# Kernel optimization log

Hardware: AMD Instinct MI355X
Metric: run time of the kernel (lower is better)

The kernel has to match this reference:

```python
import jax, jax.numpy as jnp
import numpy as np
from jax import lax

B, T, Z, H, F = 64, 256, 128, 512, 64
EPS = 1e-3  # keras LayerNormalization default epsilon


def _glorot(key, shape):
    fan_in, fan_out = shape[0], shape[1]
    lim = np.sqrt(6.0 / (fan_in + fan_out)).astype(np.float32)
    return jax.random.uniform(key, shape, jnp.float32, -lim, lim)


def setup_inputs() -> dict:
    key = jax.random.key(0)
    ks = jax.random.split(key, 16)
    inp = {
        "z": jax.random.normal(ks[0], (B, T, Z), jnp.float32),
        "Wp": _glorot(ks[1], (Z, 2 * H)), "bp": jnp.zeros((2 * H,), jnp.float32),
        "Ws": _glorot(ks[2], (Z, H)), "bs": jnp.zeros((H,), jnp.float32),
        "K0": _glorot(ks[3], (2 * H, 4 * H)), "R0": _glorot(ks[4], (H, 4 * H)), "b0": jnp.zeros((4 * H,), jnp.float32),
        "K1": _glorot(ks[5], (H, 4 * H)), "R1": _glorot(ks[6], (H, 4 * H)), "b1": jnp.zeros((4 * H,), jnp.float32),
        "K2": _glorot(ks[7], (H, 4 * H)), "R2": _glorot(ks[8], (H, 4 * H)), "b2": jnp.zeros((4 * H,), jnp.float32),
        "gamma": jnp.ones((H,), jnp.float32), "beta": jnp.zeros((H,), jnp.float32),
        "W1": _glorot(ks[9], (H, H)), "b1d": jnp.zeros((H,), jnp.float32),
        "W2": _glorot(ks[10], (H, F)), "b2d": jnp.zeros((F,), jnp.float32),
    }
    return inp


def _lstm(x, K, R, b):
    # x: [B, T, D]; keras gate order i, f, g(c), o
    xK = jnp.swapaxes(jnp.einsum('btd,dg->btg', x, K) + b, 0, 1)  # [T, B, 4H]
    h0 = jnp.zeros((x.shape[0], H), x.dtype)
    c0 = jnp.zeros((x.shape[0], H), x.dtype)

    def step(carry, xk):
        h, c = carry
        zg = xk + h @ R
        i, f, g, o = jnp.split(zg, 4, axis=-1)
        c = jax.nn.sigmoid(f) * c + jax.nn.sigmoid(i) * jnp.tanh(g)
        h = jax.nn.sigmoid(o) * jnp.tanh(c)
        return (h, c), h

    _, hs = lax.scan(step, (h0, c0), xK)
    return jnp.swapaxes(hs, 0, 1)  # [B, T, H]


def reference(z, Wp, bp, Ws, bs, K0, R0, b0, K1, R1, b1, K2, R2, b2,
              gamma, beta, W1, b1d, W2, b2d):
    x = jnp.einsum('btz,zd->btd', z, Wp) + bp          # dense_proj -> [B,T,2H]
    residual = jnp.einsum('btz,zh->bth', z, Ws) + bs   # skip_proj  -> [B,T,H]
    x = _lstm(x, K0, R0, b0)
    x = _lstm(x, K1, R1, b1)
    x = x + residual  # use_residual, after layer index 1
    x = _lstm(x, K2, R2, b2)
    # training=False: dropout is identity and attention branch is skipped
    mu = jnp.mean(x, axis=-1, keepdims=True)
    var = jnp.mean(jnp.square(x - mu), axis=-1, keepdims=True)
    x = (x - mu) * lax.rsqrt(var + EPS) * gamma + beta
    x = jax.nn.relu(jnp.einsum('bth,hk->btk', x, W1) + b1d)
    x = jnp.tanh(jnp.einsum('bth,hf->btf', x, W2) + b2d)
    return x
```

## Files before the change

kernel.cpp:

```cpp
#include <hip/hip_runtime.h>
#include <hip/hip_fp16.h>
#include <stdint.h>

typedef unsigned short u16;
typedef unsigned int   u32;
typedef unsigned long long u64;
typedef __attribute__((ext_vector_type(8))) short s16x8;
typedef __attribute__((ext_vector_type(8))) _Float16 h16x8;
typedef __attribute__((ext_vector_type(4))) float f32x4;

#define T_LEN 256

__device__ __forceinline__ u16 f2h(float f){ return __half_as_ushort(__float2half(f)); }
__device__ __forceinline__ float h2f(u16 x){ union{u16 u; _Float16 h;} c; c.u = x; return (float)c.h; }
__device__ __forceinline__ h16x8 as_h(s16x8 v){ union{s16x8 s; h16x8 h;} u; u.s=v; return u.h; }
__device__ __forceinline__ float sigm(float x){ return 1.f/(1.f + __expf(-x)); }
__device__ __forceinline__ float tanh_f(float x){ return 2.f*sigm(2.f*x) - 1.f; }

__global__ void k_fuse(const float* __restrict__ Wp, const float* __restrict__ K0,
                       const float* __restrict__ Ws, const float* __restrict__ K2,
                       float* __restrict__ Wf0, float* __restrict__ Wf2)
{
  const int c  = blockIdx.x*256 + threadIdx.x;
  const int by = blockIdx.y;
  float acc[8] = {0,0,0,0,0,0,0,0};
  if (by < 16){
    const int r0 = by*8;
    for (int d = 0; d < 1024; ++d){
      float kv = K0[(size_t)d*2048 + c];
      #pragma unroll
      for (int ii = 0; ii < 8; ++ii) acc[ii] = fmaf(Wp[(size_t)(r0+ii)*1024 + d], kv, acc[ii]);
    }
    #pragma unroll
    for (int ii = 0; ii < 8; ++ii) Wf0[(size_t)(r0+ii)*2048 + c] = acc[ii];
  } else {
    const int r0 = (by-16)*8;
    for (int u = 0; u < 512; ++u){
      float kv = K2[(size_t)u*2048 + c];
      #pragma unroll
      for (int ii = 0; ii < 8; ++ii) acc[ii] = fmaf(Ws[(size_t)(r0+ii)*512 + u], kv, acc[ii]);
    }
    #pragma unroll
    for (int ii = 0; ii < 8; ++ii) Wf2[(size_t)(r0+ii)*2048 + c] = acc[ii];
  }
}

__global__ void k_bias(const float* __restrict__ bp, const float* __restrict__ K0,
                       const float* __restrict__ b0, const float* __restrict__ bs,
                       const float* __restrict__ K2, const float* __restrict__ b2,
                       float* __restrict__ gb0, float* __restrict__ gb2)
{
  const int bx = blockIdx.x;
  if (bx < 8){
    int c = bx*256 + threadIdx.x;
    float a = b0[c];
    for (int d = 0; d < 1024; ++d) a = fmaf(bp[d], K0[(size_t)d*2048 + c], a);
    gb0[c] = a;
  } else {
    int c = (bx-8)*256 + threadIdx.x;
    float a = b2[c];
    for (int u = 0; u < 512; ++u) a = fmaf(bs[u], K2[(size_t)u*2048 + c], a);
    gb2[c] = a;
  }
}

__global__ void k_zero(u32* __restrict__ hfz, int* __restrict__ flags)
{
  int idx = blockIdx.x*256 + threadIdx.x;
  if (idx < 49152){
    int L = idx >> 14, off = idx & 16383;
    hfz[(size_t)L*257*16384 + off] = 0u;
  }
  if (blockIdx.x == 0 && threadIdx.x < 192) flags[threadIdx.x] = -1;
}

__device__ __forceinline__ size_t gidx(int k, int c, int K32c){
  int gate = c >> 9, u = c & 511;
  int jj = u >> 3, uu = u & 7;
  int lc = gate*8 + uu;
  return ((size_t)(jj*2 + (lc>>4))*K32c + (k>>5))*512
         + (size_t)((((k>>3)&3)*16 + (lc&15))*8) + (size_t)(k&7);
}
__device__ __forceinline__ size_t fidx(int k, int c){
  return ((size_t)(c>>4)*16 + (k>>5))*512
         + (size_t)((((k>>3)&3)*16 + (c&15))*8) + (size_t)(k&7);
}

__global__ void k_pack(const float* __restrict__ R0, const float* __restrict__ Wf0,
                       const float* __restrict__ R1, const float* __restrict__ K1,
                       const float* __restrict__ R2, const float* __restrict__ K2,
                       const float* __restrict__ Wf2, const float* __restrict__ W1,
                       const float* __restrict__ W2, const float* __restrict__ z,
                       u16* __restrict__ wgt0, u16* __restrict__ wgt1, u16* __restrict__ wgt2,
                       u16* __restrict__ w1p,  u16* __restrict__ w2p,  u16* __restrict__ zp)
{
  const long NT = 8159232;
  for (long i = (long)blockIdx.x*256 + threadIdx.x; i < NT; i += (long)gridDim.x*256){
    if (i < 1310720){
      int k = (int)(i >> 11), c = (int)(i & 2047);
      float v = (k < 512) ? R0[(size_t)k*2048 + c] : Wf0[(size_t)(k-512)*2048 + c];
      wgt0[gidx(k, c, 20)] = f2h(v);
    } else if (i < 3407872){
      long i2 = i - 1310720; int k = (int)(i2 >> 11), c = (int)(i2 & 2047);
      float v = (k < 512) ? R1[(size_t)k*2048 + c] : K1[(size_t)(k-512)*2048 + c];
      wgt1[gidx(k, c, 32)] = f2h(v);
    } else if (i < 5767168){
      long i2 = i - 3407872; int k = (int)(i2 >> 11), c = (int)(i2 & 2047);
      float v = (k < 512)  ? R2[(size_t)k*2048 + c]
              : (k < 1024) ? K2[(size_t)(k-512)*2048 + c]
                           : Wf2[(size_t)(k-1024)*2048 + c];
      wgt2[gidx(k, c, 36)] = f2h(v);
    } else if (i < 6029312){
      long i2 = i - 5767168; int k = (int)(i2 >> 9), c = (int)(i2 & 511);
      w1p[fidx(k, c)] = f2h(W1[(size_t)k*512 + c]);
    } else if (i < 6062080){
      long i2 = i - 6029312; int k = (int)(i2 >> 6), c = (int)(i2 & 63);
      w2p[fidx(k, c)] = f2h(W2[(size_t)k*64 + c]);
    } else {
      long i2 = i - 6062080;
      int bb = (int)(i2 >> 15), rem = (int)(i2 & 32767);
      int tt = rem >> 7, k = rem & 127;
      zp[(((size_t)tt*4 + (bb>>4))*4 + (k>>5))*512
         + (size_t)((((k>>3)&3)*16 + (bb&15))*8) + (size_t)(k&7)] = f2h(z[i2]);
    }
  }
}

__global__ __launch_bounds__(256, 1) void k_wave(
    const u16* __restrict__ wgt0, const u16* __restrict__ wgt1, const u16* __restrict__ wgt2,
    const u16* __restrict__ zp, u16* __restrict__ hf, int* flags,
    u64* __restrict__ ackdump, const float* __restrict__ gb0,
    const float* __restrict__ b1g, const float* __restrict__ gb2)
{
  __shared__ __align__(16) u16 wsm[2*36*512];
  __shared__ float zg[64][33];
  __shared__ __align__(16) u16 hsh[64][8];
  const int tid = threadIdx.x;
  const int bid = blockIdx.x;
  const int L   = bid >> 6;
  const int j   = bid & 63;
  const int K32r = (L==0) ? 20 : ((L==1) ? 32 : 36);

  { const u16* wsrc = (L==0) ? wgt0 + (size_t)j*20480
                    : (L==1) ? wgt1 + (size_t)j*32768
                             : wgt2 + (size_t)j*36864;
    const uint4* s4 = (const uint4*)wsrc; uint4* d4 = (uint4*)wsm;
    const int n4 = K32r*128;
    for (int i = tid; i < n4; i += 256) d4[i] = s4[i]; }

  const int b    = tid & 63;
  const int q    = tid >> 6;
  const int w    = q;
  const int lane = tid & 63;

  float bias[2][4];
  { const float* bsrc = (L==0) ? gb0 : (L==1) ? b1g : gb2;
    #pragma unroll
    for (int ci = 0; ci < 2; ++ci){
      int ucol = j*8 + 2*q + ci;
      #pragma unroll
      for (int g = 0; g < 4; ++g) bias[ci][g] = bsrc[g*512 + ucol];
    } }
  float cst0 = 0.f, cst1 = 0.f;
  u64 ackacc = 0;

  const int smt   = tid >> 5;
  const int sbm   = (tid >> 1) & 15;
  const int shalf = tid & 1;
  const size_t schunk = ((size_t)(smt*16 + (j>>2))*64 + ((j&3)*16 + sbm))*8 + shalf*4;

  __syncthreads();

  for (int s = 0; s < T_LEN + 2; ++s){
    if (q == 0){
      const int need = s - 1;
      int g = 0;
      for (;;){
        int okk = (__hip_atomic_load(&flags[L*64 + lane], __ATOMIC_RELAXED,
                                     __HIP_MEMORY_SCOPE_AGENT) >= need);
        if (L > 0)
          okk &= (__hip_atomic_load(&flags[(L-1)*64 + lane], __ATOMIC_RELAXED,
                                    __HIP_MEMORY_SCOPE_AGENT) >= need);
        if (__all(okk) || ++g > (1<<20)) break;
        __builtin_amdgcn_s_sleep(2);
      }
    }
    __syncthreads();

    const int t = s - L;
    if (t >= 0 && t < T_LEN){
      f32x4 acc0 = {0.f,0.f,0.f,0.f};
      f32x4 acc1 = {0.f,0.f,0.f,0.f};
      const size_t wl8 = (size_t)w*8192 + (size_t)lane*8;
      const u16* hself = hf + ((size_t)(L*257 + t))*32768 + wl8;
      const u16* hblw  = (L > 0) ? hf + ((size_t)((L-1)*257 + t + 1))*32768 + wl8 : nullptr;
      const u16* zpt   = zp + (size_t)t*8192 + (size_t)w*2048 + (size_t)lane*8;

      if (L == 0){
        s16x8 areg[20];
        #pragma unroll
        for (int kk = 0; kk < 16; ++kk) areg[kk]    = *(const s16x8*)(hself + (size_t)kk*512);
        #pragma unroll
        for (int kk = 0; kk < 4; ++kk)  areg[16+kk] = *(const s16x8*)(zpt   + (size_t)kk*512);
        #pragma unroll
        for (int kk = 0; kk < 20; ++kk){
          h16x8 bv0 = as_h(*(const s16x8*)&wsm[kk*512 + lane*8]);
          h16x8 bv1 = as_h(*(const s16x8*)&wsm[(20+kk)*512 + lane*8]);
          acc0 = __builtin_amdgcn_mfma_f32_16x16x32_f16(as_h(areg[kk]), bv0, acc0, 0, 0, 0);
          acc1 = __builtin_amdgcn_mfma_f32_16x16x32_f16(as_h(areg[kk]), bv1, acc1, 0, 0, 0);
        }
      } else if (L == 1){
        s16x8 areg[32];
        #pragma unroll
        for (int kk = 0; kk < 16; ++kk) areg[kk]    = *(const s16x8*)(hself + (size_t)kk*512);
        #pragma unroll
        for (int kk = 0; kk < 16; ++kk) areg[16+kk] = *(const s16x8*)(hblw  + (size_t)kk*512);
        #pragma unroll
        for (int kk = 0; kk < 32; ++kk){
          h16x8 bv0 = as_h(*(const s16x8*)&wsm[kk*512 + lane*8]);
          h16x8 bv1 = as_h(*(const s16x8*)&wsm[(32+kk)*512 + lane*8]);
          acc0 = __builtin_amdgcn_mfma_f32_16x16x32_f16(as_h(areg[kk]), bv0, acc0, 0, 0, 0);
          acc1 = __builtin_amdgcn_mfma_f32_16x16x32_f16(as_h(areg[kk]), bv1, acc1, 0, 0, 0);
        }
      } else {
        s16x8 areg[36];
        #pragma unroll
        for (int kk = 0; kk < 16; ++kk) areg[kk]    = *(const s16x8*)(hself + (size_t)kk*512);
        #pragma unroll
        for (int kk = 0; kk < 16; ++kk) areg[16+kk] = *(const s16x8*)(hblw  + (size_t)kk*512);
        #pragma unroll
        for (int kk = 0; kk < 4; ++kk)  areg[32+kk] = *(const s16x8*)(zpt   + (size_t)kk*512);
        #pragma unroll
        for (int kk = 0; kk < 36; ++kk){
          h16x8 bv0 = as_h(*(const s16x8*)&wsm[kk*512 + lane*8]);
          h16x8 bv1 = as_h(*(const s16x8*)&wsm[(36+kk)*512 + lane*8]);
          acc0 = __builtin_amdgcn_mfma_f32_16x16x32_f16(as_h(areg[kk]), bv0, acc0, 0, 0, 0);
          acc1 = __builtin_amdgcn_mfma_f32_16x16x32_f16(as_h(areg[kk]), bv1, acc1, 0, 0, 0);
        }
      }
      #pragma unroll
      for (int r = 0; r < 4; ++r){
        int row = (w << 4) + ((lane >> 4) << 2) + r;
        zg[row][lane & 15]        = acc0[r];
        zg[row][16 + (lane & 15)] = acc1[r];
      }
      __syncthreads();

      float hv0, hv1;
      {
        int uu = 2*q;
        float zi = zg[b][uu]      + bias[0][0];
        float zf = zg[b][8 + uu]  + bias[0][1];
        float zc = zg[b][16 + uu] + bias[0][2];
        float zo = zg[b][24 + uu] + bias[0][3];
        float cc = sigm(zf)*cst0 + sigm(zi)*tanh_f(zc);
        cst0 = cc; hv0 = sigm(zo)*tanh_f(cc);
      }
      {
        int uu = 2*q + 1;
        float zi = zg[b][uu]      + bias[1][0];
        float zf = zg[b][8 + uu]  + bias[1][1];
        float zc = zg[b][16 + uu] + bias[1][2];
        float zo = zg[b][24 + uu] + bias[1][3];
        float cc = sigm(zf)*cst1 + sigm(zi)*tanh_f(zc);
        cst1 = cc; hv1 = sigm(zo)*tanh_f(cc);
      }
      *(u32*)&hsh[b][2*q] = (u32)f2h(hv0) | ((u32)f2h(hv1) << 16);
      __syncthreads();
      if (tid < 128){
        u16* hdst = hf + ((size_t)(L*257 + t + 1))*32768;
        u64 v = *(const u64*)&hsh[smt*16 + sbm][shalf*4];
        u64 old = __hip_atomic_exchange((u64*)(hdst + schunk), v,
                                        __ATOMIC_RELAXED, __HIP_MEMORY_SCOPE_AGENT);
        ackacc ^= old;
      }
    }
    __syncthreads();
    if (tid == 0)
      __hip_atomic_store(&flags[L*64 + j], s, __ATOMIC_RELAXED, __HIP_MEMORY_SCOPE_AGENT);
  }
  if (tid < 128) ackdump[((size_t)bid << 7) + tid] = ackacc;
}

__global__ __launch_bounds__(256) void k_ep(
    const u16* __restrict__ hf, const float* __restrict__ gam, const float* __restrict__ bet,
    const u16* __restrict__ w1p, const u16* __restrict__ w2p,
    const float* __restrict__ b1d, const float* __restrict__ b2d, float* __restrict__ out)
{
  __shared__ __align__(16) u16 xs[32768];
  __shared__ __align__(16) u16 yf[32768];
  __shared__ float redS[64][8];
  __shared__ float muS[64], rsS[64];
  const int t = blockIdx.x, tid = threadIdx.x;

  { const uint4* src = (const uint4*)(hf + ((size_t)(2*257 + t + 1))*32768);
    uint4* dst = (uint4*)xs;
    #pragma unroll
    for (int i = 0; i < 16; ++i) dst[tid + 256*i] = src[tid + 256*i]; }
  __syncthreads();

  const int r = tid >> 2, qq = tid & 3;
  const int mt = r >> 4, ml = r & 15;
  float sum = 0.f, sq = 0.f;
  #pragma unroll
  for (int k32 = qq*4; k32 < qq*4 + 4; ++k32)
    #pragma unroll
    for (int kq = 0; kq < 4; ++kq){
      s16x8 v = *(const s16x8*)&xs[(((mt*16 + k32)*64) + kq*16 + ml)*8];
      #pragma unroll
      for (int e = 0; e < 8; ++e){
        float x = h2f(((const u16*)&v)[e]);
        sum += x; sq += x*x;
      }
    }
  redS[r][qq] = sum; redS[r][4+qq] = sq;
  __syncthreads();
  if (qq == 0){
    float s1 = redS[r][0]+redS[r][1]+redS[r][2]+redS[r][3];
    float s2 = redS[r][4]+redS[r][5]+redS[r][6]+redS[r][7];
    float m  = s1 * (1.f/512.f);
    float var = s2 * (1.f/512.f) - m*m;
    muS[r] = m; rsS[r] = rsqrtf(var + 1e-3f);
  }
  __syncthreads();
  { const float m = muS[r], rstd = rsS[r];
    #pragma unroll
    for (int k32 = qq*4; k32 < qq*4 + 4; ++k32)
      #pragma unroll
      for (int kq = 0; kq < 4; ++kq){
        u16* pp = &xs[(((mt*16 + k32)*64) + kq*16 + ml)*8];
        s16x8 v = *(const s16x8*)pp;
        #pragma unroll
        for (int e = 0; e < 8; ++e){
          int k = k32*32 + kq*8 + e;
          float xn = (h2f(((const u16*)&v)[e]) - m)*rstd*gam[k] + bet[k];
          pp[e] = f2h(xn);
        }
      } }
  __syncthreads();

  const int w = tid >> 6, lane = tid & 63;
  f32x4 acc[4][8];
  f32x4 vz = {0.f,0.f,0.f,0.f};
  #pragma unroll
  for (int a = 0; a < 4; ++a)
    #pragma unroll
    for (int n = 0; n < 8; ++n) acc[a][n] = vz;
  for (int k32 = 0; k32 < 16; ++k32){
    h16x8 av[4];
    #pragma unroll
    for (int mt2 = 0; mt2 < 4; ++mt2) av[mt2] = as_h(*(const s16x8*)&xs[((mt2*16 + k32)*64 + lane)*8]);
    #pragma unroll
    for (int nn = 0; nn < 8; ++nn){
      const int n16 = w*8 + nn;
      h16x8 bv = as_h(*(const s16x8*)&w1p[((size_t)(n16*16 + k32)*64 + lane)*8]);
      #pragma unroll
      for (int mt2 = 0; mt2 < 4; ++mt2)
        acc[mt2][nn] = __builtin_amdgcn_mfma_f32_16x16x32_f16(av[mt2], bv, acc[mt2][nn], 0,0,0);
    }
  }
  #pragma unroll
  for (int nn = 0; nn < 8; ++nn){
    int col = (w*8 + nn)*16 + (lane & 15);
    float bv = b1d[col];
    #pragma unroll
    for (int mt2 = 0; mt2 < 4; ++mt2){
      #pragma unroll
      for (int rr = 0; rr < 4; ++rr){
        int row = mt2*16 + ((lane >> 4) << 2) + rr;
        float v = acc[mt2][nn][rr] + bv;
        v = fmaxf(v, 0.f);
        yf[((mt2*16 + (col>>5))*64 + ((col>>3)&3)*16 + (row&15))*8 + (col&7)] = f2h(v);
      } } }
  __syncthreads();

  f32x4 acc2[4];
  #pragma unroll
  for (int mt2 = 0; mt2 < 4; ++mt2) acc2[mt2] = vz;
  for (int k32 = 0; k32 < 16; ++k32){
    h16x8 bv = as_h(*(const s16x8*)&w2p[((size_t)(w*16 + k32)*64 + lane)*8]);
    #pragma unroll
    for (int mt2 = 0; mt2 < 4; ++mt2){
      h16x8 av = as_h(*(const s16x8*)&yf[((mt2*16 + k32)*64 + lane)*8]);
      acc2[mt2] = __builtin_amdgcn_mfma_f32_16x16x32_f16(av, bv, acc2[mt2], 0,0,0);
    } }
  const int f = w*16 + (lane & 15);
  const float bf_ = b2d[f];
  #pragma unroll
  for (int mt2 = 0; mt2 < 4; ++mt2)
    #pragma unroll
    for (int rr = 0; rr < 4; ++rr){
      int row = mt2*16 + ((lane >> 4) << 2) + rr;
      out[((size_t)row*T_LEN + t)*64 + f] = tanh_f(acc2[mt2][rr] + bf_);
    }
}

extern "C" void kernel_launch(void* const* d_in, const int* in_sizes, int n_in,
                              void* d_out, int out_size, void* d_ws, size_t ws_size,
                              hipStream_t stream)
{
  const float* z    = (const float*)d_in[0];
  const float* Wp   = (const float*)d_in[1];
  const float* bp   = (const float*)d_in[2];
  const float* Ws   = (const float*)d_in[3];
  const float* bs   = (const float*)d_in[4];
  const float* K0   = (const float*)d_in[5];
  const float* R0   = (const float*)d_in[6];
  const float* b0   = (const float*)d_in[7];
  const float* K1   = (const float*)d_in[8];
  const float* R1   = (const float*)d_in[9];
  const float* b1   = (const float*)d_in[10];
  const float* K2   = (const float*)d_in[11];
  const float* R2   = (const float*)d_in[12];
  const float* b2   = (const float*)d_in[13];
  const float* gam  = (const float*)d_in[14];
  const float* bet  = (const float*)d_in[15];
  const float* W1   = (const float*)d_in[16];
  const float* b1d  = (const float*)d_in[17];
  const float* W2   = (const float*)d_in[18];
  const float* b2d  = (const float*)d_in[19];
  float* out = (float*)d_out;
  (void)in_sizes; (void)n_in; (void)out_size; (void)ws_size;

  char* base = (char*)d_ws;
  size_t off = 0;
  auto carve = [&](size_t bytes)->char* {
    char* p = base + off;
    off = (off + bytes + 255) & ~(size_t)255;
    return p;
  };
  u16*   wgt0 = (u16*)  carve((size_t)64*20480*2);
  u16*   wgt1 = (u16*)  carve((size_t)64*32768*2);
  u16*   wgt2 = (u16*)  carve((size_t)64*36864*2);
  u16*   w1p  = (u16*)  carve((size_t)262144*2);
  u16*   w2p  = (u16*)  carve((size_t)32768*2);
  u16*   zp   = (u16*)  carve((size_t)2097152*2);
  float* Wf0  = (float*)carve((size_t)262144*4);
  float* Wf2  = (float*)carve((size_t)262144*4);
  float* gb0  = (float*)carve((size_t)2048*4);
  float* gb2  = (float*)carve((size_t)2048*4);
  u16*   hf   = (u16*)  carve((size_t)3*257*32768*2);
  int*   flags= (int*)  carve((size_t)1024);
  u64*   ackd = (u64*)  carve((size_t)192*128*8);

  k_fuse<<<dim3(8,32), dim3(256), 0, stream>>>(Wp, K0, Ws, K2, Wf0, Wf2);
  k_bias<<<dim3(16),   dim3(256), 0, stream>>>(bp, K0, b0, bs, K2, b2, gb0, gb2);
  k_zero<<<dim3(768),  dim3(256), 0, stream>>>((u32*)hf, flags);
  k_pack<<<dim3(4096), dim3(256), 0, stream>>>(R0, Wf0, R1, K1, R2, K2, Wf2, W1, W2, z,
                                               wgt0, wgt1, wgt2, w1p, w2p, zp);
  k_wave<<<dim3(192),  dim3(256), 0, stream>>>(wgt0, wgt1, wgt2, zp, hf, flags,
                                               ackd, gb0, b1, gb2);
  k_ep<<<dim3(256),    dim3(256), 0, stream>>>(hf, gam, bet, w1p, w2p, b1d, b2d, out);
}
```

Measured before the change: 1.930 ms.

## Replace per-step barrier flag store with per-wave counter increments and skewed layer pipeline

The single end-of-step flag store, which needed a block-wide barrier, is replaced by two waves that each atomically increment a counter after their own writes drain. Waiting now happens only on active steps, with a two-step skew between layers and a shorter sleep. The h-history slots are permuted through a scrambled slot index, apparently to spread writes across memory channels. Scheduling barriers after the A-operand loads keep the loads grouped ahead of the MFMA loop. The counter protocol is more intricate and relies on vmcnt waits to order the data writes before the flag increment.

```diff
diff --git a/kernel.cpp b/kernel.cpp
--- a/kernel.cpp
+++ b/kernel.cpp
@@ -16,6 +16,8 @@
 __device__ __forceinline__ h16x8 as_h(s16x8 v){ union{s16x8 s; h16x8 h;} u; u.s=v; return u.h; }
 __device__ __forceinline__ float sigm(float x){ return 1.f/(1.f + __expf(-x)); }
 __device__ __forceinline__ float tanh_f(float x){ return 2.f*sigm(2.f*x) - 1.f; }
+
+__device__ __forceinline__ int slotid(int t){ return (t < 0) ? 256 : ((t*151) & 255); }
 
 __global__ void k_fuse(const float* __restrict__ Wp, const float* __restrict__ K0,
                        const float* __restrict__ Ws, const float* __restrict__ K2,
@@ -69,9 +71,9 @@
   int idx = blockIdx.x*256 + threadIdx.x;
   if (idx < 49152){
     int L = idx >> 14, off = idx & 16383;
-    hfz[(size_t)L*257*16384 + off] = 0u;
-  }
-  if (blockIdx.x == 0 && threadIdx.x < 192) flags[threadIdx.x] = -1;
+    hfz[((size_t)L*257 + 256)*16384 + off] = 0u;
+  }
+  if (blockIdx.x == 0 && threadIdx.x < 192) flags[threadIdx.x] = 0;
 }
 
 __device__ __forceinline__ size_t gidx(int k, int c, int K32c){
@@ -164,36 +166,38 @@
   float cst0 = 0.f, cst1 = 0.f;
   u64 ackacc = 0;
 
-  const int smt   = tid >> 5;
-  const int sbm   = (tid >> 1) & 15;
-  const int shalf = tid & 1;
+  const int pid   = tid - 128;
+  const int smt   = pid >> 5;
+  const int sbm   = (pid >> 1) & 15;
+  const int shalf = pid & 1;
   const size_t schunk = ((size_t)(smt*16 + (j>>2))*64 + ((j&3)*16 + sbm))*8 + shalf*4;
 
   __syncthreads();
 
-  for (int s = 0; s < T_LEN + 2; ++s){
-    if (q == 0){
-      const int need = s - 1;
+  for (int s = 0; s < T_LEN + 4; ++s){
+    const int t = s - 2*L;
+    if (q == 0 && t >= 0 && t < T_LEN){
+      const int needS = 2*s;
+      const int needB = 2*(s-1);
       int g = 0;
       for (;;){
         int okk = (__hip_atomic_load(&flags[L*64 + lane], __ATOMIC_RELAXED,
-                                     __HIP_MEMORY_SCOPE_AGENT) >= need);
+                                     __HIP_MEMORY_SCOPE_AGENT) >= needS);
         if (L > 0)
           okk &= (__hip_atomic_load(&flags[(L-1)*64 + lane], __ATOMIC_RELAXED,
-                                    __HIP_MEMORY_SCOPE_AGENT) >= need);
+                                    __HIP_MEMORY_SCOPE_AGENT) >= needB);
         if (__all(okk) || ++g > (1<<20)) break;
-        __builtin_amdgcn_s_sleep(2);
+        __builtin_amdgcn_s_sleep(1);
       }
     }
     __syncthreads();
 
-    const int t = s - L;
     if (t >= 0 && t < T_LEN){
       f32x4 acc0 = {0.f,0.f,0.f,0.f};
       f32x4 acc1 = {0.f,0.f,0.f,0.f};
       const size_t wl8 = (size_t)w*8192 + (size_t)lane*8;
-      const u16* hself = hf + ((size_t)(L*257 + t))*32768 + wl8;
-      const u16* hblw  = (L > 0) ? hf + ((size_t)((L-1)*257 + t + 1))*32768 + wl8 : nullptr;
+      const u16* hself = hf + ((size_t)(L*257 + slotid(t-1)))*32768 + wl8;
+      const u16* hblw  = (L > 0) ? hf + ((size_t)((L-1)*257 + slotid(t)))*32768 + wl8 : nullptr;
       const u16* zpt   = zp + (size_t)t*8192 + (size_t)w*2048 + (size_t)lane*8;
 
       if (L == 0){
@@ -202,6 +206,7 @@
         for (int kk = 0; kk < 16; ++kk) areg[kk]    = *(const s16x8*)(hself + (size_t)kk*512);
         #pragma unroll
         for (int kk = 0; kk < 4; ++kk)  areg[16+kk] = *(const s16x8*)(zpt   + (size_t)kk*512);
+        __builtin_amdgcn_sched_barrier(0);
         #pragma unroll
         for (int kk = 0; kk < 20; ++kk){
           h16x8 bv0 = as_h(*(const s16x8*)&wsm[kk*512 + lane*8]);
@@ -215,6 +220,7 @@
         for (int kk = 0; kk < 16; ++kk) areg[kk]    = *(const s16x8*)(hself + (size_t)kk*512);
         #pragma unroll
         for (int kk = 0; kk < 16; ++kk) areg[16+kk] = *(const s16x8*)(hblw  + (size_t)kk*512);
+        __builtin_amdgcn_sched_barrier(0);
         #pragma unroll
         for (int kk = 0; kk < 32; ++kk){
           h16x8 bv0 = as_h(*(const s16x8*)&wsm[kk*512 + lane*8]);
@@ -230,6 +236,7 @@
         for (int kk = 0; kk < 16; ++kk) areg[16+kk] = *(const s16x8*)(hblw  + (size_t)kk*512);
         #pragma unroll
         for (int kk = 0; kk < 4; ++kk)  areg[32+kk] = *(const s16x8*)(zpt   + (size_t)kk*512);
+        __builtin_amdgcn_sched_barrier(0);
         #pragma unroll
         for (int kk = 0; kk < 36; ++kk){
           h16x8 bv0 = as_h(*(const s16x8*)&wsm[kk*512 + lane*8]);
@@ -267,17 +274,24 @@
       }
       *(u32*)&hsh[b][2*q] = (u32)f2h(hv0) | ((u32)f2h(hv1) << 16);
       __syncthreads();
-      if (tid < 128){
-        u16* hdst = hf + ((size_t)(L*257 + t + 1))*32768;
+
+      if (tid >= 128){
+        u16* hdst = hf + ((size_t)(L*257 + slotid(t)))*32768;
         u64 v = *(const u64*)&hsh[smt*16 + sbm][shalf*4];
         u64 old = __hip_atomic_exchange((u64*)(hdst + schunk), v,
                                         __ATOMIC_RELAXED, __HIP_MEMORY_SCOPE_AGENT);
         ackacc ^= old;
-      }
-    }
-    __syncthreads();
-    if (tid == 0)
-      __hip_atomic_store(&flags[L*64 + j], s, __ATOMIC_RELAXED, __HIP_MEMORY_SCOPE_AGENT);
+        asm volatile("s_waitcnt vmcnt(0)" ::: "memory");
+        __builtin_amdgcn_sched_barrier(0);
+        if ((tid & 63) == 0)
+          __hip_atomic_fetch_add(&flags[L*64 + j], 1, __ATOMIC_RELAXED,
+                                 __HIP_MEMORY_SCOPE_AGENT);
+      }
+    } else {
+      if (tid >= 128 && (tid & 63) == 0)
+        __hip_atomic_fetch_add(&flags[L*64 + j], 1, __ATOMIC_RELAXED,
+                               __HIP_MEMORY_SCOPE_AGENT);
+    }
   }
   if (tid < 128) ackdump[((size_t)bid << 7) + tid] = ackacc;
 }
@@ -293,7 +307,7 @@
   __shared__ float muS[64], rsS[64];
   const int t = blockIdx.x, tid = threadIdx.x;
 
-  { const uint4* src = (const uint4*)(hf + ((size_t)(2*257 + t + 1))*32768);
+  { const uint4* src = (const uint4*)(hf + ((size_t)(2*257 + slotid(t)))*32768);
     uint4* dst = (uint4*)xs;
     #pragma unroll
     for (int i = 0; i < 16; ++i) dst[tid + 256*i] = src[tid + 256*i]; }
```

New measurement: 2.076 ms. +7.6%, slower.
